# Optimization experiments

Hardware: AMD Instinct MI355X
Metric: run time of the kernel (lower is better)

## Reference

```python
import jax, jax.numpy as jnp
import numpy as np

N_NODES = 100000
N_EDGES = 1600000
IN_C, HID_C, OUT_C = 128, 128, 64


def gcn_conv(x, src, dst, W, b, num_nodes):
    # PyG GCNConv: add self-loops, symmetric normalization, linear transform,
    # aggregate source features into targets.
    h = x @ W  # [N, C_out]
    loop = jnp.arange(num_nodes, dtype=src.dtype)
    s = jnp.concatenate([src, loop])
    d = jnp.concatenate([dst, loop])
    deg = jax.ops.segment_sum(jnp.ones_like(d, dtype=h.dtype), d, num_segments=num_nodes)
    inv_sqrt = jnp.where(deg > 0, jax.lax.rsqrt(deg), 0.0)
    norm = inv_sqrt[s] * inv_sqrt[d]  # [E+N]
    msgs = h[s] * norm[:, None]  # gather + scale
    out = jax.ops.segment_sum(msgs, d, num_segments=num_nodes)  # scatter-add
    return out + b


def setup_inputs() -> dict:
    key = jax.random.key(0)
    k1, k2, k3, k4 = jax.random.split(key, 4)
    x = jax.random.normal(k1, (N_NODES, IN_C), dtype=jnp.float32)
    edge_index = jax.random.randint(k2, (2, N_EDGES), 0, N_NODES, dtype=jnp.int64)
    W1 = jax.random.normal(k3, (IN_C, HID_C), dtype=jnp.float32) * (1.0 / np.sqrt(IN_C))
    b1 = jnp.zeros((HID_C,), dtype=jnp.float32)
    W2 = jax.random.normal(k4, (HID_C, OUT_C), dtype=jnp.float32) * (1.0 / np.sqrt(HID_C))
    b2 = jnp.zeros((OUT_C,), dtype=jnp.float32)
    return {"x": x, "edge_index": edge_index, "W1": W1, "b1": b1, "W2": W2, "b2": b2}


def reference(x, edge_index, W1, b1, W2, b2):
    num_nodes = x.shape[0]
    src, dst = edge_index[0], edge_index[1]  # PyG flow: source -> target
    h = gcn_conv(x, src, dst, W1, b1, num_nodes)
    h = jax.nn.relu(h)  # dropout is identity in eval mode
    out = gcn_conv(h, src, dst, W2, b2, num_nodes)
    return out
```

## Files before the change

### kernel.cpp

```cpp
#include <hip/hip_runtime.h>

#define IN_C 128
#define HID_C 128
#define OUT_C 64

#define BSPAN 256
#define BCAP  5120
#define NBMAX 512
#define ACHUNK 4096

typedef unsigned int uint32;
typedef unsigned short ushort16;
typedef _Float16 f16;
typedef f16   f16x8 __attribute__((ext_vector_type(8)));
typedef float f32x4 __attribute__((ext_vector_type(4)));


__device__ __forceinline__ ushort16 f2bf(float f) {
    union { float f; uint32 u; } v; v.f = f;
    uint32 r = v.u + 0x7FFFu + ((v.u >> 16) & 1u);
    return (ushort16)(r >> 16);
}

__device__ __forceinline__ void unpack2(uint32 u, float& f0, float& f1) {
    union { uint32 x; float f; } a, b;
    a.x = u << 16;
    b.x = u & 0xFFFF0000u;
    f0 = a.f; f1 = b.f;
}

__device__ __forceinline__ void acc_row(uint4 r, float* acc) {
    float f0, f1;
    unpack2(r.x, f0, f1); acc[0] += f0; acc[1] += f1;
    unpack2(r.y, f0, f1); acc[2] += f0; acc[3] += f1;
    unpack2(r.z, f0, f1); acc[4] += f0; acc[5] += f1;
    unpack2(r.w, f0, f1); acc[6] += f0; acc[7] += f1;
}


__launch_bounds__(256)
__global__ void bin_edges_kernel(const int* __restrict__ src, const int* __restrict__ dst,
                                 int* __restrict__ bucketCur, uint32* __restrict__ binned,
                                 int E, int nbuck) {
    __shared__ int hist[NBMAX];
    __shared__ int base[NBMAX];
    const int tid = threadIdx.x;
    const int e0  = blockIdx.x * ACHUNK;

    for (int i = tid; i < NBMAX; i += 256) hist[i] = 0;
    __syncthreads();

    int d[16], s[16], rk[16];
#pragma unroll
    for (int j = 0; j < 16; j++) {
        int e = e0 + j * 256 + tid;
        if (e < E) {
            d[j] = dst[e];
            s[j] = src[e];
            rk[j] = atomicAdd(&hist[d[j] >> 8], 1);
        } else d[j] = -1;
    }
    __syncthreads();

    for (int b = tid; b < nbuck; b += 256) {
        int h = hist[b];
        base[b] = h ? atomicAdd(&bucketCur[b], h) : 0;
    }
    __syncthreads();

#pragma unroll
    for (int j = 0; j < 16; j++) {
        if (d[j] >= 0) {
            int b = d[j] >> 8;
            int pos = base[b] + rk[j];
            if (pos < BCAP)
                binned[(size_t)b * BCAP + pos] =
                    ((uint32)(d[j] & 255) << 17) | (uint32)s[j];
        }
    }
}


__launch_bounds__(256)
__global__ void bucket_csr_kernel(const uint32* __restrict__ binned,
                                  const int* __restrict__ bucketCur,
                                  int* __restrict__ csr_src, int* __restrict__ rowbeg,
                                  int* __restrict__ rowend, float* __restrict__ inv, int N) {
    constexpr int MAXIT = BCAP / 256;
    __shared__ int cnt[BSPAN];
    __shared__ int scn[BSPAN];
    __shared__ int excl[BSPAN];
    const int b   = blockIdx.x;
    const int tid = threadIdx.x;
    const int n0  = b * BSPAN;
    const int ne  = min(bucketCur[b], BCAP);
    const uint32* bp = binned + (size_t)b * BCAP;

    cnt[tid] = 0;
    __syncthreads();

    uint32 ebuf[MAXIT];
    int    rbuf[MAXIT];
    int nmine = 0;
    for (int i = tid; i < ne; i += 256) {
        uint32 e = bp[i];
        ebuf[nmine] = e;
        rbuf[nmine] = atomicAdd(&cnt[e >> 17], 1);
        nmine++;
    }
    __syncthreads();

    int v = cnt[tid];
    scn[tid] = v;
    __syncthreads();
    for (int off = 1; off < 256; off <<= 1) {
        int u = (tid >= off) ? scn[tid - off] : 0;
        __syncthreads();
        scn[tid] += u;
        __syncthreads();
    }
    int ex = scn[tid] - v;
    excl[tid] = ex;

    int n = n0 + tid;
    if (n < N) {
        int gb = b * BCAP + ex;
        rowbeg[n] = gb;
        rowend[n] = gb + v;
        inv[n] = rsqrtf((float)(v + 1));
    }
    __syncthreads();

    for (int j = 0; j < nmine; j++) {
        uint32 e = ebuf[j];
        csr_src[(size_t)b * BCAP + excl[e >> 17] + rbuf[j]] = (int)(e & 0x1FFFFu);
    }
}


template <int C>
__device__ __forceinline__ void wprep_one(const float* __restrict__ W, f16* __restrict__ Wf, int t) {
    constexpr int NCT = C / 16;
    int lane = t & 63;
    int ctkc = t >> 6;
    int ct = ctkc % NCT, kc = ctkc / NCT;
    int kbase = kc * 32 + (lane >> 4) * 8;
    int col   = ct * 16 + (lane & 15);
    f16 v[8];
#pragma unroll
    for (int j = 0; j < 8; j++) v[j] = (f16)W[(size_t)(kbase + j) * C + col];
    *(uint4*)(Wf + (size_t)t * 8) = *(const uint4*)v;
}

__global__ void wprep_both(const float* __restrict__ W1, f16* __restrict__ Wf1,
                           const float* __restrict__ W2, f16* __restrict__ Wf2,
                           int* __restrict__ bucketCur, int nbuck) {
    constexpr int T1 = 4 * (HID_C / 16) * 64;
    constexpr int T2 = 4 * (OUT_C / 16) * 64;
    int t = blockIdx.x * 256 + threadIdx.x;
    if (t < nbuck) bucketCur[t] = 0;
    if (t < T1)            wprep_one<HID_C>(W1, Wf1, t);
    else if (t < T1 + T2)  wprep_one<OUT_C>(W2, Wf2, t - T1);
}


template <int C>
__launch_bounds__(256)
__global__ void mfma_gemm(const float* __restrict__ X, const f16* __restrict__ Wf,
                          const float* __restrict__ inv, ushort16* __restrict__ outb, int N) {
    constexpr int NCT = C / 16;
    __shared__ __align__(16) f16 As[4 * 4 * 64 * 8];
    __shared__ __align__(16) f16 Bs[4 * NCT * 64 * 8];

    const int tid  = threadIdx.x;
    const int lane = tid & 63;
    const int w    = tid >> 6;
    const int row0 = blockIdx.x * 64;

    {
        constexpr int TOT = 4 * NCT * 64 * 8;
        const uint4* src = (const uint4*)Wf;
        uint4* dst = (uint4*)Bs;
#pragma unroll
        for (int i = 0; i < TOT / 8 / 256; i++)
            dst[tid + i * 256] = src[tid + i * 256];
    }

    {
        int r   = tid >> 2;
        int seg = tid & 3;
        int row = row0 + r;
        int ws_ = r >> 4;
        int r15 = r & 15;
#pragma unroll
        for (int i = 0; i < 8; i++) {
            int k = seg * 32 + i * 4;
            float4 v = make_float4(0.f, 0.f, 0.f, 0.f);
            if (row < N) v = *(const float4*)(X + (size_t)row * 128 + k);
            int q = (k >> 3) & 3, j0 = k & 7;
            f16 h[4] = {(f16)v.x, (f16)v.y, (f16)v.z, (f16)v.w};
            int slot = ((seg * 4 + ws_) * 64 + (q * 16 + r15)) * 8 + j0;
            *(uint2*)(As + slot) = *(const uint2*)h;
        }
    }
    __syncthreads();

    f32x4 acc[NCT];
#pragma unroll
    for (int c = 0; c < NCT; c++) acc[c] = (f32x4){0.f, 0.f, 0.f, 0.f};
#pragma unroll
    for (int kc = 0; kc < 4; kc++) {
        f16x8 a = *(const f16x8*)&As[((kc * 4 + w) * 64 + lane) * 8];
#pragma unroll
        for (int ct = 0; ct < NCT; ct++) {
            f16x8 b = *(const f16x8*)&Bs[((kc * NCT + ct) * 64 + lane) * 8];
            acc[ct] = __builtin_amdgcn_mfma_f32_16x16x32_f16(a, b, acc[ct], 0, 0, 0);
        }
    }

    __syncthreads();
    ushort16* Ds = (ushort16*)As;
    const int q = lane >> 4;
    float iv[4];
#pragma unroll
    for (int reg = 0; reg < 4; reg++) {
        int row = row0 + w * 16 + q * 4 + reg;
        iv[reg] = (row < N) ? inv[row] : 0.f;
    }
#pragma unroll
    for (int ct = 0; ct < NCT; ct++) {
#pragma unroll
        for (int reg = 0; reg < 4; reg++) {
            int r = w * 16 + q * 4 + reg;
            Ds[r * C + ct * 16 + (lane & 15)] = f2bf(acc[ct][reg] * iv[reg]);
        }
    }
    __syncthreads();
    {
        int r  = tid >> 2;
        int row = row0 + r;
        if (row < N) {
            constexpr int SPT = C / 4;
            int c0 = (tid & 3) * SPT;
            const uint4* s = (const uint4*)&Ds[r * C + c0];
            uint4* d = (uint4*)(outb + (size_t)row * C + c0);
#pragma unroll
            for (int i = 0; i < SPT / 8; i++) d[i] = s[i];
        }
    }
}


__launch_bounds__(512, 4)
__global__ void fused_gather_gemm(const int* __restrict__ rowbeg, const int* __restrict__ rowend,
                                  const int* __restrict__ csr,
                                  const ushort16* __restrict__ hsb,
                                  const float* __restrict__ inv, const float* __restrict__ bias1,
                                  const f16* __restrict__ Wf2,
                                  ushort16* __restrict__ outb, int N) {
    constexpr int CIN = 128, COUT = 64, NCT = COUT / 16;
    __shared__ __align__(16) f16 As[4 * 4 * 64 * 8];
    __shared__ __align__(16) f16 Bs[4 * NCT * 64 * 8];

    const int tid  = threadIdx.x;
    const int lane = tid & 63;
    const int w    = tid >> 6;
    const int row0 = blockIdx.x * 64;

    {
        const uint4* s = (const uint4*)Wf2;
        uint4* d = (uint4*)Bs;
        d[tid]       = s[tid];
        d[tid + 512] = s[tid + 512];
    }

    {
        const int r = tid >> 3;
        const int q = tid & 7;
        const int n = row0 + r;
        float acc[16];
#pragma unroll
        for (int j = 0; j < 16; j++) acc[j] = 0.f;

        if (n < N) {
            {
                const ushort16* base = hsb + (size_t)n * CIN + q * 16;
                uint4 s0 = *(const uint4*)(base);
                uint4 s1 = *(const uint4*)(base + 8);
                acc_row(s0, acc); acc_row(s1, acc + 8);
            }
            const int end = rowend[n];
            int i = rowbeg[n];
            for (; i + 4 <= end; i += 4) {
                const ushort16* p0 = hsb + (size_t)csr[i]     * CIN + q * 16;
                const ushort16* p1 = hsb + (size_t)csr[i + 1] * CIN + q * 16;
                const ushort16* p2 = hsb + (size_t)csr[i + 2] * CIN + q * 16;
                const ushort16* p3 = hsb + (size_t)csr[i + 3] * CIN + q * 16;
                uint4 a0 = *(const uint4*)(p0);
                uint4 a1 = *(const uint4*)(p0 + 8);
                uint4 b0 = *(const uint4*)(p1);
                uint4 b1 = *(const uint4*)(p1 + 8);
                uint4 c0 = *(const uint4*)(p2);
                uint4 c1 = *(const uint4*)(p2 + 8);
                uint4 d0 = *(const uint4*)(p3);
                uint4 d1 = *(const uint4*)(p3 + 8);
                acc_row(a0, acc); acc_row(a1, acc + 8);
                acc_row(b0, acc); acc_row(b1, acc + 8);
                acc_row(c0, acc); acc_row(c1, acc + 8);
                acc_row(d0, acc); acc_row(d1, acc + 8);
            }
            for (; i < end; i++) {
                const ushort16* p0 = hsb + (size_t)csr[i] * CIN + q * 16;
                uint4 a0 = *(const uint4*)(p0);
                uint4 a1 = *(const uint4*)(p0 + 8);
                acc_row(a0, acc); acc_row(a1, acc + 8);
            }

            float iv = inv[n];
#pragma unroll
            for (int j = 0; j < 16; j++)
                acc[j] = fmaxf(fmaf(iv, acc[j], bias1[q * 16 + j]), 0.f);
        }

        const int ws_ = r >> 4, r15 = r & 15;
        const int seg = q >> 1;
#pragma unroll
        for (int u = 0; u < 2; u++) {
            const int i8 = (q & 1) * 2 + u;
            f16 hv[8];
#pragma unroll
            for (int j = 0; j < 8; j++) hv[j] = (f16)acc[u * 8 + j];
            int slot = ((seg * 4 + ws_) * 64 + (i8 * 16 + r15)) * 8;
            *(uint4*)(As + slot) = *(const uint4*)hv;
        }
    }
    __syncthreads();

    f32x4 acc2[NCT];
#pragma unroll
    for (int c = 0; c < NCT; c++) acc2[c] = (f32x4){0.f, 0.f, 0.f, 0.f};
    if (w < 4) {
#pragma unroll
        for (int kc = 0; kc < 4; kc++) {
            f16x8 a = *(const f16x8*)&As[((kc * 4 + w) * 64 + lane) * 8];
#pragma unroll
            for (int ct = 0; ct < NCT; ct++) {
                f16x8 b = *(const f16x8*)&Bs[((kc * NCT + ct) * 64 + lane) * 8];
                acc2[ct] = __builtin_amdgcn_mfma_f32_16x16x32_f16(a, b, acc2[ct], 0, 0, 0);
            }
        }
    }

    __syncthreads();
    ushort16* Ds = (ushort16*)As;
    if (w < 4) {
        const int q2 = lane >> 4;
        float iv2[4];
#pragma unroll
        for (int reg = 0; reg < 4; reg++) {
            int row = row0 + w * 16 + q2 * 4 + reg;
            iv2[reg] = (row < N) ? inv[row] : 0.f;
        }
#pragma unroll
        for (int ct = 0; ct < NCT; ct++) {
#pragma unroll
            for (int reg = 0; reg < 4; reg++) {
                int r = w * 16 + q2 * 4 + reg;
                Ds[r * COUT + ct * 16 + (lane & 15)] = f2bf(acc2[ct][reg] * iv2[reg]);
            }
        }
    }
    __syncthreads();
    {
        const int r   = tid >> 3;
        const int row = row0 + r;
        if (row < N) {
            const int c0 = (tid & 7) * 8;
            *(uint4*)(outb + (size_t)row * COUT + c0) = *(const uint4*)&Ds[r * COUT + c0];
        }
    }
}


template <int C, bool RELU>
__launch_bounds__(256)
__global__ void gather_agg_bf16(const int* __restrict__ rowbeg, const int* __restrict__ rowend,
                                const int* __restrict__ csr_src,
                                const ushort16* __restrict__ hsb, const float* __restrict__ inv,
                                const float* __restrict__ b, float* __restrict__ out, int N) {
    constexpr int TPN = C / 8;
    constexpr int NPB = 256 / TPN;
    int n    = blockIdx.x * NPB + threadIdx.x / TPN;
    int lane = threadIdx.x % TPN;
    if (n >= N) return;
    int c8 = lane * 8;

    float acc[8];
    {
        uint4 raw = *(const uint4*)(hsb + (size_t)n * C + c8);
        unpack2(raw.x, acc[0], acc[1]);
        unpack2(raw.y, acc[2], acc[3]);
        unpack2(raw.z, acc[4], acc[5]);
        unpack2(raw.w, acc[6], acc[7]);
    }

    int beg = rowbeg[n];
    int end = rowend[n];
    int i = beg;
    for (; i + 4 <= end; i += 4) {
        int s0 = csr_src[i];
        int s1 = csr_src[i + 1];
        int s2 = csr_src[i + 2];
        int s3 = csr_src[i + 3];
        uint4 r0 = *(const uint4*)(hsb + (size_t)s0 * C + c8);
        uint4 r1 = *(const uint4*)(hsb + (size_t)s1 * C + c8);
        uint4 r2 = *(const uint4*)(hsb + (size_t)s2 * C + c8);
        uint4 r3 = *(const uint4*)(hsb + (size_t)s3 * C + c8);
        acc_row(r0, acc); acc_row(r1, acc); acc_row(r2, acc); acc_row(r3, acc);
    }
    for (; i < end; i++) {
        uint4 r0 = *(const uint4*)(hsb + (size_t)csr_src[i] * C + c8);
        acc_row(r0, acc);
    }

    float iv = inv[n];
    float4 b0 = *(const float4*)(b + c8);
    float4 b1 = *(const float4*)(b + c8 + 4);
    float r[8];
    r[0] = fmaf(iv, acc[0], b0.x); r[1] = fmaf(iv, acc[1], b0.y);
    r[2] = fmaf(iv, acc[2], b0.z); r[3] = fmaf(iv, acc[3], b0.w);
    r[4] = fmaf(iv, acc[4], b1.x); r[5] = fmaf(iv, acc[5], b1.y);
    r[6] = fmaf(iv, acc[6], b1.z); r[7] = fmaf(iv, acc[7], b1.w);
    if (RELU) {
#pragma unroll
        for (int j = 0; j < 8; j++) r[j] = fmaxf(r[j], 0.f);
    }
    float* po = out + (size_t)n * C + c8;
    *(float4*)(po)     = make_float4(r[0], r[1], r[2], r[3]);
    *(float4*)(po + 4) = make_float4(r[4], r[5], r[6], r[7]);
}

extern "C" void kernel_launch(void* const* d_in, const int* in_sizes, int n_in,
                              void* d_out, int out_size, void* d_ws, size_t ws_size,
                              hipStream_t stream) {
    const float* x  = (const float*)d_in[0];
    const int*   ei = (const int*)d_in[1];
    const float* W1 = (const float*)d_in[2];
    const float* b1 = (const float*)d_in[3];
    const float* W2 = (const float*)d_in[4];
    const float* b2 = (const float*)d_in[5];
    float* out = (float*)d_out;

    const int N = in_sizes[0] / IN_C;
    const int E = in_sizes[1] / 2;
    const int* src = ei;
    const int* dst = ei + E;
    const int nbuck = (N + BSPAN - 1) / BSPAN;

    char* ws = (char*)d_ws;
    auto align_up = [](size_t v) { return (v + 1023) & ~(size_t)1023; };
    size_t off = 0;
    int*      bucketCur = (int*)(ws + off);      off += align_up((size_t)nbuck * sizeof(int));
    float*    inv       = (float*)(ws + off);    off += align_up((size_t)N * sizeof(float));
    int*      rowbeg    = (int*)(ws + off);      off += align_up((size_t)N * sizeof(int));
    int*      rowend    = (int*)(ws + off);      off += align_up((size_t)N * sizeof(int));
    uint32*   binned    = (uint32*)(ws + off);   off += align_up((size_t)nbuck * BCAP * sizeof(uint32));
    int*      csrs      = (int*)(ws + off);      off += align_up((size_t)nbuck * BCAP * sizeof(int));
    f16*      Wf1       = (f16*)(ws + off);      off += align_up((size_t)4 * (HID_C/16) * 64 * 8 * sizeof(f16));
    f16*      Wf2       = (f16*)(ws + off);      off += align_up((size_t)4 * (OUT_C/16) * 64 * 8 * sizeof(f16));
    ushort16* hs1b      = (ushort16*)(ws + off); off += align_up((size_t)N * HID_C * sizeof(ushort16));
    ushort16* hs2b      = (ushort16*)(ws + off); off += align_up((size_t)N * OUT_C * sizeof(ushort16));

    wprep_both<<<(4 * (HID_C/16 + OUT_C/16) * 64 + 255) / 256, 256, 0, stream>>>(
        W1, Wf1, W2, Wf2, bucketCur, nbuck);
    bin_edges_kernel<<<(E + ACHUNK - 1) / ACHUNK, 256, 0, stream>>>(
        src, dst, bucketCur, binned, E, nbuck);
    bucket_csr_kernel<<<nbuck, 256, 0, stream>>>(
        binned, bucketCur, csrs, rowbeg, rowend, inv, N);

    mfma_gemm<HID_C><<<(N + 63) / 64, 256, 0, stream>>>(x, Wf1, inv, hs1b, N);

    fused_gather_gemm<<<(N + 63) / 64, 512, 0, stream>>>(
        rowbeg, rowend, csrs, hs1b, inv, b1, Wf2, hs2b, N);

    {
        constexpr int NPB = 256 / (OUT_C / 8);
        gather_agg_bf16<OUT_C, false><<<(N + NPB - 1) / NPB, 256, 0, stream>>>(
            rowbeg, rowend, csrs, hs2b, inv, b2, out, N);
    }
}
```

Measured before the change: 259.0 us.

## Merge CSR build and first GEMM into one launch using global-atomic degrees

Per-node degrees are now counted with global atomics in the edge-binning kernel, so the first-layer GEMM no longer depends on the CSR kernel's inv array. The bucket CSR construction and the layer-1 MFMA GEMM are merged into a single launch, with separate block ranges doing each job so they run concurrently and one kernel launch is removed. In exchange, 1.6M global atomics on scattered degree counters are added to the binning kernel, and the wprep kernel is widened to zero the degree array.

```diff
diff --git a/kernel.cpp b/kernel.cpp
--- a/kernel.cpp
+++ b/kernel.cpp
@@ -41,7 +41,7 @@
 __launch_bounds__(256)
 __global__ void bin_edges_kernel(const int* __restrict__ src, const int* __restrict__ dst,
                                  int* __restrict__ bucketCur, uint32* __restrict__ binned,
-                                 int E, int nbuck) {
+                                 int* __restrict__ deg, int E, int nbuck) {
     __shared__ int hist[NBMAX];
     __shared__ int base[NBMAX];
     const int tid = threadIdx.x;
@@ -58,6 +58,7 @@
             d[j] = dst[e];
             s[j] = src[e];
             rk[j] = atomicAdd(&hist[d[j] >> 8], 1);
+            atomicAdd(&deg[d[j]], 1);
         } else d[j] = -1;
     }
     __syncthreads();
@@ -77,63 +78,6 @@
                 binned[(size_t)b * BCAP + pos] =
                     ((uint32)(d[j] & 255) << 17) | (uint32)s[j];
         }
-    }
-}
-
-
-__launch_bounds__(256)
-__global__ void bucket_csr_kernel(const uint32* __restrict__ binned,
-                                  const int* __restrict__ bucketCur,
-                                  int* __restrict__ csr_src, int* __restrict__ rowbeg,
-                                  int* __restrict__ rowend, float* __restrict__ inv, int N) {
-    constexpr int MAXIT = BCAP / 256;
-    __shared__ int cnt[BSPAN];
-    __shared__ int scn[BSPAN];
-    __shared__ int excl[BSPAN];
-    const int b   = blockIdx.x;
-    const int tid = threadIdx.x;
-    const int n0  = b * BSPAN;
-    const int ne  = min(bucketCur[b], BCAP);
-    const uint32* bp = binned + (size_t)b * BCAP;
-
-    cnt[tid] = 0;
-    __syncthreads();
-
-    uint32 ebuf[MAXIT];
-    int    rbuf[MAXIT];
-    int nmine = 0;
-    for (int i = tid; i < ne; i += 256) {
-        uint32 e = bp[i];
-        ebuf[nmine] = e;
-        rbuf[nmine] = atomicAdd(&cnt[e >> 17], 1);
-        nmine++;
-    }
-    __syncthreads();
-
-    int v = cnt[tid];
-    scn[tid] = v;
-    __syncthreads();
-    for (int off = 1; off < 256; off <<= 1) {
-        int u = (tid >= off) ? scn[tid - off] : 0;
-        __syncthreads();
-        scn[tid] += u;
-        __syncthreads();
-    }
-    int ex = scn[tid] - v;
-    excl[tid] = ex;
-
-    int n = n0 + tid;
-    if (n < N) {
-        int gb = b * BCAP + ex;
-        rowbeg[n] = gb;
-        rowend[n] = gb + v;
-        inv[n] = rsqrtf((float)(v + 1));
-    }
-    __syncthreads();
-
-    for (int j = 0; j < nmine; j++) {
-        uint32 e = ebuf[j];
-        csr_src[(size_t)b * BCAP + excl[e >> 17] + rbuf[j]] = (int)(e & 0x1FFFFu);
     }
 }
 
@@ -154,98 +98,157 @@
 
 __global__ void wprep_both(const float* __restrict__ W1, f16* __restrict__ Wf1,
                            const float* __restrict__ W2, f16* __restrict__ Wf2,
-                           int* __restrict__ bucketCur, int nbuck) {
+                           int* __restrict__ bucketCur, int* __restrict__ deg,
+                           int nbuck, int N) {
     constexpr int T1 = 4 * (HID_C / 16) * 64;
     constexpr int T2 = 4 * (OUT_C / 16) * 64;
     int t = blockIdx.x * 256 + threadIdx.x;
     if (t < nbuck) bucketCur[t] = 0;
+    if (t < N)     deg[t] = 0;
     if (t < T1)            wprep_one<HID_C>(W1, Wf1, t);
     else if (t < T1 + T2)  wprep_one<OUT_C>(W2, Wf2, t - T1);
 }
 
 
-template <int C>
 __launch_bounds__(256)
-__global__ void mfma_gemm(const float* __restrict__ X, const f16* __restrict__ Wf,
-                          const float* __restrict__ inv, ushort16* __restrict__ outb, int N) {
-    constexpr int NCT = C / 16;
-    __shared__ __align__(16) f16 As[4 * 4 * 64 * 8];
-    __shared__ __align__(16) f16 Bs[4 * NCT * 64 * 8];
-
-    const int tid  = threadIdx.x;
-    const int lane = tid & 63;
-    const int w    = tid >> 6;
-    const int row0 = blockIdx.x * 64;
-
-    {
-        constexpr int TOT = 4 * NCT * 64 * 8;
-        const uint4* src = (const uint4*)Wf;
-        uint4* dst = (uint4*)Bs;
-#pragma unroll
-        for (int i = 0; i < TOT / 8 / 256; i++)
-            dst[tid + i * 256] = src[tid + i * 256];
-    }
-
-    {
-        int r   = tid >> 2;
-        int seg = tid & 3;
-        int row = row0 + r;
-        int ws_ = r >> 4;
-        int r15 = r & 15;
-#pragma unroll
-        for (int i = 0; i < 8; i++) {
-            int k = seg * 32 + i * 4;
-            float4 v = make_float4(0.f, 0.f, 0.f, 0.f);
-            if (row < N) v = *(const float4*)(X + (size_t)row * 128 + k);
-            int q = (k >> 3) & 3, j0 = k & 7;
-            f16 h[4] = {(f16)v.x, (f16)v.y, (f16)v.z, (f16)v.w};
-            int slot = ((seg * 4 + ws_) * 64 + (q * 16 + r15)) * 8 + j0;
-            *(uint2*)(As + slot) = *(const uint2*)h;
-        }
-    }
-    __syncthreads();
-
-    f32x4 acc[NCT];
-#pragma unroll
-    for (int c = 0; c < NCT; c++) acc[c] = (f32x4){0.f, 0.f, 0.f, 0.f};
-#pragma unroll
-    for (int kc = 0; kc < 4; kc++) {
-        f16x8 a = *(const f16x8*)&As[((kc * 4 + w) * 64 + lane) * 8];
+__global__ void csr_and_gemm(const uint32* __restrict__ binned, const int* __restrict__ bucketCur,
+                             int* __restrict__ csr_src, int* __restrict__ rowbeg,
+                             int* __restrict__ rowend, float* __restrict__ inv,
+                             const float* __restrict__ X, const f16* __restrict__ Wf,
+                             const int* __restrict__ deg, ushort16* __restrict__ outb,
+                             int N, int ncsr) {
+    __shared__ __align__(16) char smem[49152];
+    const int tid = threadIdx.x;
+
+    if ((int)blockIdx.x < ncsr) {
+        constexpr int MAXIT = BCAP / 256;
+        int* cnt  = (int*)smem;
+        int* scn  = cnt + BSPAN;
+        int* excl = scn + BSPAN;
+        const int b   = blockIdx.x;
+        const int n0  = b * BSPAN;
+        const int ne  = min(bucketCur[b], BCAP);
+        const uint32* bp = binned + (size_t)b * BCAP;
+
+        cnt[tid] = 0;
+        __syncthreads();
+
+        uint32 ebuf[MAXIT];
+        int    rbuf[MAXIT];
+        int nmine = 0;
+        for (int i = tid; i < ne; i += 256) {
+            uint32 e = bp[i];
+            ebuf[nmine] = e;
+            rbuf[nmine] = atomicAdd(&cnt[e >> 17], 1);
+            nmine++;
+        }
+        __syncthreads();
+
+        int v = cnt[tid];
+        scn[tid] = v;
+        __syncthreads();
+        for (int off = 1; off < 256; off <<= 1) {
+            int u = (tid >= off) ? scn[tid - off] : 0;
+            __syncthreads();
+            scn[tid] += u;
+            __syncthreads();
+        }
+        int ex = scn[tid] - v;
+        excl[tid] = ex;
+
+        int n = n0 + tid;
+        if (n < N) {
+            int gb = b * BCAP + ex;
+            rowbeg[n] = gb;
+            rowend[n] = gb + v;
+            inv[n] = rsqrtf((float)(v + 1));
+        }
+        __syncthreads();
+
+        for (int j = 0; j < nmine; j++) {
+            uint32 e = ebuf[j];
+            csr_src[(size_t)b * BCAP + excl[e >> 17] + rbuf[j]] = (int)(e & 0x1FFFFu);
+        }
+    } else {
+        constexpr int C = HID_C;
+        constexpr int NCT = C / 16;
+        f16* As = (f16*)smem;
+        f16* Bs = (f16*)(smem + 16384);
+
+        const int lane = tid & 63;
+        const int w    = tid >> 6;
+        const int row0 = ((int)blockIdx.x - ncsr) * 64;
+
+        {
+            constexpr int TOT = 4 * NCT * 64 * 8;
+            const uint4* s = (const uint4*)Wf;
+            uint4* d = (uint4*)Bs;
+#pragma unroll
+            for (int i = 0; i < TOT / 8 / 256; i++)
+                d[tid + i * 256] = s[tid + i * 256];
+        }
+
+        {
+            int r   = tid >> 2;
+            int seg = tid & 3;
+            int row = row0 + r;
+            int ws_ = r >> 4;
+            int r15 = r & 15;
+#pragma unroll
+            for (int i = 0; i < 8; i++) {
+                int k = seg * 32 + i * 4;
+                float4 v = make_float4(0.f, 0.f, 0.f, 0.f);
+                if (row < N) v = *(const float4*)(X + (size_t)row * 128 + k);
+                int q = (k >> 3) & 3, j0 = k & 7;
+                f16 h[4] = {(f16)v.x, (f16)v.y, (f16)v.z, (f16)v.w};
+                int slot = ((seg * 4 + ws_) * 64 + (q * 16 + r15)) * 8 + j0;
+                *(uint2*)(As + slot) = *(const uint2*)h;
+            }
+        }
+        __syncthreads();
+
+        f32x4 acc[NCT];
+#pragma unroll
+        for (int c = 0; c < NCT; c++) acc[c] = (f32x4){0.f, 0.f, 0.f, 0.f};
+#pragma unroll
+        for (int kc = 0; kc < 4; kc++) {
+            f16x8 a = *(const f16x8*)&As[((kc * 4 + w) * 64 + lane) * 8];
+#pragma unroll
+            for (int ct = 0; ct < NCT; ct++) {
+                f16x8 b = *(const f16x8*)&Bs[((kc * NCT + ct) * 64 + lane) * 8];
+                acc[ct] = __builtin_amdgcn_mfma_f32_16x16x32_f16(a, b, acc[ct], 0, 0, 0);
+            }
+        }
+
+        __syncthreads();
+        ushort16* Ds = (ushort16*)As;
+        const int q = lane >> 4;
+        float iv[4];
+#pragma unroll
+        for (int reg = 0; reg < 4; reg++) {
+            int row = row0 + w * 16 + q * 4 + reg;
+            iv[reg] = (row < N) ? rsqrtf((float)(deg[row] + 1)) : 0.f;
+        }
 #pragma unroll
         for (int ct = 0; ct < NCT; ct++) {
-            f16x8 b = *(const f16x8*)&Bs[((kc * NCT + ct) * 64 + lane) * 8];
-            acc[ct] = __builtin_amdgcn_mfma_f32_16x16x32_f16(a, b, acc[ct], 0, 0, 0);
-        }
-    }
-
-    __syncthreads();
-    ushort16* Ds = (ushort16*)As;
-    const int q = lane >> 4;
-    float iv[4];
-#pragma unroll
-    for (int reg = 0; reg < 4; reg++) {
-        int row = row0 + w * 16 + q * 4 + reg;
-        iv[reg] = (row < N) ? inv[row] : 0.f;
-    }
-#pragma unroll
-    for (int ct = 0; ct < NCT; ct++) {
-#pragma unroll
-        for (int reg = 0; reg < 4; reg++) {
-            int r = w * 16 + q * 4 + reg;
-            Ds[r * C + ct * 16 + (lane & 15)] = f2bf(acc[ct][reg] * iv[reg]);
-        }
-    }
-    __syncthreads();
-    {
-        int r  = tid >> 2;
-        int row = row0 + r;
-        if (row < N) {
-            constexpr int SPT = C / 4;
-            int c0 = (tid & 3) * SPT;
-            const uint4* s = (const uint4*)&Ds[r * C + c0];
-            uint4* d = (uint4*)(outb + (size_t)row * C + c0);
-#pragma unroll
-            for (int i = 0; i < SPT / 8; i++) d[i] = s[i];
+#pragma unroll
+            for (int reg = 0; reg < 4; reg++) {
+                int r = w * 16 + q * 4 + reg;
+                Ds[r * C + ct * 16 + (lane & 15)] = f2bf(acc[ct][reg] * iv[reg]);
+            }
+        }
+        __syncthreads();
+        {
+            int r  = tid >> 2;
+            int row = row0 + r;
+            if (row < N) {
+                constexpr int SPT = C / 4;
+                int c0 = (tid & 3) * SPT;
+                const uint4* s = (const uint4*)&Ds[r * C + c0];
+                uint4* d = (uint4*)(outb + (size_t)row * C + c0);
+#pragma unroll
+                for (int i = 0; i < SPT / 8; i++) d[i] = s[i];
+            }
         }
     }
 }
@@ -461,6 +464,7 @@
     auto align_up = [](size_t v) { return (v + 1023) & ~(size_t)1023; };
     size_t off = 0;
     int*      bucketCur = (int*)(ws + off);      off += align_up((size_t)nbuck * sizeof(int));
+    int*      deg       = (int*)(ws + off);      off += align_up((size_t)N * sizeof(int));
     float*    inv       = (float*)(ws + off);    off += align_up((size_t)N * sizeof(float));
     int*      rowbeg    = (int*)(ws + off);      off += align_up((size_t)N * sizeof(int));
     int*      rowend    = (int*)(ws + off);      off += align_up((size_t)N * sizeof(int));
@@ -471,14 +475,18 @@
     ushort16* hs1b      = (ushort16*)(ws + off); off += align_up((size_t)N * HID_C * sizeof(ushort16));
     ushort16* hs2b      = (ushort16*)(ws + off); off += align_up((size_t)N * OUT_C * sizeof(ushort16));
 
-    wprep_both<<<(4 * (HID_C/16 + OUT_C/16) * 64 + 255) / 256, 256, 0, stream>>>(
-        W1, Wf1, W2, Wf2, bucketCur, nbuck);
+    wprep_both<<<(N + 255) / 256, 256, 0, stream>>>(
+        W1, Wf1, W2, Wf2, bucketCur, deg, nbuck, N);
+
     bin_edges_kernel<<<(E + ACHUNK - 1) / ACHUNK, 256, 0, stream>>>(
-        src, dst, bucketCur, binned, E, nbuck);
-    bucket_csr_kernel<<<nbuck, 256, 0, stream>>>(
-        binned, bucketCur, csrs, rowbeg, rowend, inv, N);
-
-    mfma_gemm<HID_C><<<(N + 63) / 64, 256, 0, stream>>>(x, Wf1, inv, hs1b, N);
+        src, dst, bucketCur, binned, deg, E, nbuck);
+
+    {
+        const int ngemm = (N + 63) / 64;
+        csr_and_gemm<<<nbuck + ngemm, 256, 0, stream>>>(
+            binned, bucketCur, csrs, rowbeg, rowend, inv,
+            x, Wf1, deg, hs1b, N, nbuck);
+    }
 
     fused_gather_gemm<<<(N + 63) / 64, 512, 0, stream>>>(
         rowbeg, rowend, csrs, hs1b, inv, b1, Wf2, hs2b, N);
```

Measured after the change: 304.5 us. 1.18x slower.
